# Kernel tuning notes

Hardware: AMD Instinct MI355X
Metric: run time of the kernel (lower is better)

The kernel has to match this reference:

```python
import jax, jax.numpy as jnp
import numpy as np

B, N, D = 256, 50, 128
N_NODE, MAX_ATTR = 50000, 2000
ALPHA = 0.2  # LeakyReLU negative slope
STDV = 1.0 / np.sqrt(D)  # reset_parameters uniform(-stdv, stdv)
NEG = -9e15


def setup_inputs() -> dict:
    key = jax.random.key(0)
    ks = jax.random.split(key, 10)
    uni = lambda k, shp: jax.random.uniform(k, shp, jnp.float32, -STDV, STDV)
    return {
        "inputs": jax.random.randint(ks[0], (B, N), 0, N_NODE),
        "adj": jax.random.randint(ks[1], (B, N, N), 0, 5),
        "mask_item": jax.random.randint(ks[2], (B, N), 0, 2),
        "A_attr_sess": jax.random.normal(ks[3], (B, MAX_ATTR), jnp.float32),
        "embedding": uni(ks[4], (N_NODE, D)),
        "attr_embedding": uni(ks[5], (MAX_ATTR, D)),
        "a0": uni(ks[6], (D,)),
        "a1": uni(ks[7], (D,)),
        "a2": uni(ks[8], (D,)),
        "a3": uni(ks[9], (D,)),
    }


def reference(inputs, adj, mask_item, A_attr_sess, embedding, attr_embedding, a0, a1, a2, a3):
    h = embedding[inputs]  # [B, N, D]
    # (h.repeat(1,1,N) * h.repeat(1,N,1)).view(B,N,N,D) == outer elementwise product h_i * h_j
    a_in = jax.nn.leaky_relu(h[:, :, None, :] * h[:, None, :, :], ALPHA)  # [B,N,N,D]
    a_all = jnp.stack([a0, a1, a2, a3], axis=-1)  # [D, 4]
    e = jnp.einsum('bijd,dk->bijk', a_in, a_all)  # [B,N,N,4]
    alpha = jnp.full(adj.shape, NEG, dtype=e.dtype)
    alpha = jnp.where(adj == 1, e[..., 0], alpha)
    alpha = jnp.where(adj == 2, e[..., 1], alpha)
    alpha = jnp.where(adj == 3, e[..., 2], alpha)
    alpha = jnp.where(adj == 4, e[..., 3], alpha)
    alpha = jax.nn.softmax(alpha, axis=-1)
    output = jnp.einsum('bij,bjd->bid', alpha, h)  # [B, N, D]
    attr_sess = A_attr_sess @ attr_embedding  # [B, D]
    return output, attr_sess
```

## Files before the change

### kernel.cpp

```cpp
#include <hip/hip_runtime.h>
#include <math.h>

#define BB 256
#define NN 50
#define DD 128
#define MAXA 2000
#define NEGV -9e15f
#define NATTR 256

#define H_S   136
#define HT_S  72
#define AL_S  72

#define H_OFF   0
#define HT_OFF  (64 * H_S)
#define AL_OFF  (HT_OFF + 128 * HT_S)
#define ADJ_OFF (AL_OFF + 64 * AL_S)
#define LDS_US  (ADJ_OFF + 64 * 64)

typedef __attribute__((ext_vector_type(8))) short        s8b;
typedef __attribute__((ext_vector_type(4))) float        f32x4;
typedef __attribute__((ext_vector_type(4))) unsigned int u32x4;

static __device__ __forceinline__ unsigned int pack2(float lo, float hi) {
    unsigned int r;
    asm("v_cvt_pk_bf16_f32 %0, %1, %2" : "=v"(r) : "v"(lo), "v"(hi));
    return r;
}
static __device__ __forceinline__ float bf2f(unsigned int s) {
    return __uint_as_float(s << 16);
}
static __device__ __forceinline__ f32x4 mfma16(u32x4 a, u32x4 b, f32x4 c) {
    return __builtin_amdgcn_mfma_f32_16x16x32_bf16(
        __builtin_bit_cast(s8b, a), __builtin_bit_cast(s8b, b), c, 0, 0, 0);
}

__global__ __launch_bounds__(256) void sg_fused_kernel(
    const int* __restrict__ inputs,
    const int* __restrict__ adj,
    const float* __restrict__ A_attr,
    const float* __restrict__ embedding,
    const float* __restrict__ attr_emb,
    const float* __restrict__ a0,
    const float* __restrict__ a1,
    const float* __restrict__ a2,
    const float* __restrict__ a3,
    float* __restrict__ out,
    float* __restrict__ ws)
{
    __shared__ __align__(16) unsigned short sh[LDS_US];
    const int blk  = blockIdx.x;
    const int tid  = threadIdx.x;
    const int w    = tid >> 6;
    const int lane = tid & 63;
    const int g    = lane >> 4;
    const int c    = lane & 15;
    const int goff = g * 8;

    if (blk < BB) {
        const int b = blk;

        const int  i_   = lane;
        const bool live = (i_ < NN);
        int node = 0;
        if (live) node = inputs[b * NN + i_];
        float4 gv[8];
        #pragma unroll
        for (int n = 0; n < 8; ++n) {
            gv[n] = make_float4(0.f, 0.f, 0.f, 0.f);
            if (live) gv[n] = *(const float4*)(embedding + (size_t)node * DD + (w * 8 + n) * 4);
        }
        for (int idx = tid; idx < 4096; idx += 256) {
            const int i = idx >> 6, j = idx & 63;
            int a = 0;
            if (i < NN && j < NN) a = adj[(size_t)b * (NN * NN) + i * NN + j];
            sh[ADJ_OFF + idx] = (unsigned short)a;
        }
        #pragma unroll
        for (int n = 0; n < 8; ++n) {
            const int d4 = w * 8 + n;
            const unsigned int pk01 = pack2(gv[n].x, gv[n].y);
            const unsigned int pk23 = pack2(gv[n].z, gv[n].w);
            *(uint2*)(sh + H_OFF + i_ * H_S + d4 * 4) = make_uint2(pk01, pk23);
            sh[HT_OFF + (d4 * 4 + 0) * HT_S + i_] = (unsigned short)pk01;
            sh[HT_OFF + (d4 * 4 + 1) * HT_S + i_] = (unsigned short)(pk01 >> 16);
            sh[HT_OFF + (d4 * 4 + 2) * HT_S + i_] = (unsigned short)pk23;
            sh[HT_OFF + (d4 * 4 + 3) * HT_S + i_] = (unsigned short)(pk23 >> 16);
        }
        __syncthreads();

        u32x4 hA[4];
        #pragma unroll
        for (int dt = 0; dt < 4; ++dt)
            hA[dt] = *(const u32x4*)(const void*)(sh + H_OFF + (w * 16 + c) * H_S + dt * 32 + goff);

        f32x4 accS[4][4];
        #pragma unroll
        for (int jt = 0; jt < 4; ++jt)
            #pragma unroll
            for (int k = 0; k < 4; ++k) accS[jt][k] = (f32x4){0.f, 0.f, 0.f, 0.f};

        #pragma unroll
        for (int dt = 0; dt < 4; ++dt) {
            float hf8[8], hb8[8];
            #pragma unroll
            for (int p = 0; p < 4; ++p) {
                const unsigned int hp = hA[dt][p];
                hf8[2 * p]     = bf2f(hp & 0xffffu);
                hf8[2 * p + 1] = bf2f(hp >> 16);
                hb8[2 * p]     = fabsf(hf8[2 * p]);
                hb8[2 * p + 1] = fabsf(hf8[2 * p + 1]);
            }
            u32x4 U[4], V[4];
            #pragma unroll
            for (int k = 0; k < 4; ++k) {
                const float* ap = (k == 0) ? a0 : (k == 1) ? a1 : (k == 2) ? a2 : a3;
                const float4 aL = *(const float4*)(ap + dt * 32 + goff);
                const float4 aH = *(const float4*)(ap + dt * 32 + goff + 4);
                const float a8[8] = {aL.x, aL.y, aL.z, aL.w, aH.x, aH.y, aH.z, aH.w};
                #pragma unroll
                for (int p = 0; p < 4; ++p) {
                    U[k][p] = pack2(0.6f * a8[2 * p] * hf8[2 * p],
                                    0.6f * a8[2 * p + 1] * hf8[2 * p + 1]);
                    V[k][p] = pack2(0.4f * a8[2 * p] * hb8[2 * p],
                                    0.4f * a8[2 * p + 1] * hb8[2 * p + 1]);
                }
            }
            #pragma unroll
            for (int jt = 0; jt < 4; ++jt) {
                const u32x4 hB = *(const u32x4*)(const void*)(sh + H_OFF + (jt * 16 + c) * H_S + dt * 32 + goff);
                u32x4 hBa;
                #pragma unroll
                for (int p = 0; p < 4; ++p) hBa[p] = hB[p] & 0x7fff7fffu;
                #pragma unroll
                for (int k = 0; k < 4; ++k) {
                    accS[jt][k] = mfma16(U[k], hB,  accS[jt][k]);
                    accS[jt][k] = mfma16(V[k], hBa, accS[jt][k]);
                }
            }
        }

        float s_[4][4];
        #pragma unroll
        for (int jt = 0; jt < 4; ++jt) {
            #pragma unroll
            for (int reg = 0; reg < 4; ++reg) {
                const int il = w * 16 + g * 4 + reg;
                const int j  = jt * 16 + c;
                const int a  = (int)sh[ADJ_OFF + il * 64 + j];
                float sv = (a == 1) ? accS[jt][0][reg] : (a == 2) ? accS[jt][1][reg]
                         : (a == 3) ? accS[jt][2][reg] : (a == 4) ? accS[jt][3][reg] : NEGV;
                if (j >= NN) sv = -INFINITY;
                s_[jt][reg] = sv;
            }
        }
        #pragma unroll
        for (int reg = 0; reg < 4; ++reg) {
            float m = fmaxf(fmaxf(s_[0][reg], s_[1][reg]), fmaxf(s_[2][reg], s_[3][reg]));
            m = fmaxf(m, __shfl_xor(m, 1));
            m = fmaxf(m, __shfl_xor(m, 2));
            m = fmaxf(m, __shfl_xor(m, 4));
            m = fmaxf(m, __shfl_xor(m, 8));
            const float p0 = __expf(s_[0][reg] - m);
            const float p1 = __expf(s_[1][reg] - m);
            const float p2 = __expf(s_[2][reg] - m);
            const float p3 = __expf(s_[3][reg] - m);
            float sum = (p0 + p1) + (p2 + p3);
            sum += __shfl_xor(sum, 1);
            sum += __shfl_xor(sum, 2);
            sum += __shfl_xor(sum, 4);
            sum += __shfl_xor(sum, 8);
            const float r  = 1.0f / sum;
            const int  il  = w * 16 + g * 4 + reg;
            sh[AL_OFF + il * AL_S +  0 + c] = (unsigned short)pack2(p0 * r, p0 * r);
            sh[AL_OFF + il * AL_S + 16 + c] = (unsigned short)pack2(p1 * r, p1 * r);
            sh[AL_OFF + il * AL_S + 32 + c] = (unsigned short)pack2(p2 * r, p2 * r);
            sh[AL_OFF + il * AL_S + 48 + c] = (unsigned short)pack2(p3 * r, p3 * r);
        }

        const int il = w * 16 + c;
        const u32x4 pa0 = *(const u32x4*)(const void*)(sh + AL_OFF + il * AL_S + goff);
        const u32x4 pa1 = *(const u32x4*)(const void*)(sh + AL_OFF + il * AL_S + 32 + goff);
        #pragma unroll
        for (int nt = 0; nt < 8; ++nt) {
            const u32x4 v0 = *(const u32x4*)(const void*)(sh + HT_OFF + (nt * 16 + c) * HT_S + goff);
            const u32x4 v1 = *(const u32x4*)(const void*)(sh + HT_OFF + (nt * 16 + c) * HT_S + 32 + goff);
            f32x4 accp = (f32x4){0.f, 0.f, 0.f, 0.f};
            accp = mfma16(pa0, v0, accp);
            accp = mfma16(pa1, v1, accp);
            #pragma unroll
            for (int reg = 0; reg < 4; ++reg) {
                const int ig = w * 16 + g * 4 + reg;
                if (ig < NN)
                    out[((size_t)b * NN + ig) * DD + nt * 16 + c] = accp[reg];
            }
        }
    } else {
        const int ablk = blk - BB;
        const int mg = ablk >> 4;
        const int ks = ablk & 15;
        const int m0 = mg * 16;
        const int wd = w * 32;
        const float* Arow = A_attr + (size_t)(m0 + c) * MAXA;

        const int k0 = (ks +  0) * 32;
        const int k1 = (ks + 16) * 32;
        const int k2 = (ks + 32) * 32;
        const int k3 = (ks + 48) * 32;
        const bool has3 = (ks < 15);
        const bool gd3  = (ks == 14);

        const float4 aL0 = *(const float4*)(Arow + k0 + goff);
        const float4 aH0 = *(const float4*)(Arow + k0 + goff + 4);
        const float4 aL1 = *(const float4*)(Arow + k1 + goff);
        const float4 aH1 = *(const float4*)(Arow + k1 + goff + 4);
        const float4 aL2 = *(const float4*)(Arow + k2 + goff);
        const float4 aH2 = *(const float4*)(Arow + k2 + goff + 4);
        float4 aL3 = make_float4(0.f, 0.f, 0.f, 0.f);
        float4 aH3 = make_float4(0.f, 0.f, 0.f, 0.f);
        if (has3) {
            if (!gd3 || k3 + goff + 3 < MAXA) aL3 = *(const float4*)(Arow + k3 + goff);
            if (!gd3 || k3 + goff + 7 < MAXA) aH3 = *(const float4*)(Arow + k3 + goff + 4);
        }
        float ev0[2][8], ev1[2][8], ev2[2][8], ev3[2][8];
        #pragma unroll
        for (int ntl = 0; ntl < 2; ++ntl) {
            const int col = wd + ntl * 16 + c;
            #pragma unroll
            for (int p = 0; p < 8; ++p) {
                ev0[ntl][p] = attr_emb[(size_t)(k0 + goff + p) * DD + col];
                ev1[ntl][p] = attr_emb[(size_t)(k1 + goff + p) * DD + col];
                ev2[ntl][p] = attr_emb[(size_t)(k2 + goff + p) * DD + col];
                const int kr = k3 + goff + p;
                ev3[ntl][p] = (has3 && (!gd3 || kr < MAXA))
                                  ? attr_emb[(size_t)kr * DD + col] : 0.f;
            }
        }
        f32x4 acc2[2];
        acc2[0] = (f32x4){0.f, 0.f, 0.f, 0.f};
        acc2[1] = (f32x4){0.f, 0.f, 0.f, 0.f};
        #define ATTR_CHUNK(AL, AH, EV)                                              \
        {                                                                           \
            u32x4 af;                                                               \
            af[0] = pack2(AL.x, AL.y); af[1] = pack2(AL.z, AL.w);                   \
            af[2] = pack2(AH.x, AH.y); af[3] = pack2(AH.z, AH.w);                   \
            _Pragma("unroll")                                                       \
            for (int ntl = 0; ntl < 2; ++ntl) {                                     \
                u32x4 bf_;                                                          \
                bf_[0] = pack2(EV[ntl][0], EV[ntl][1]);                             \
                bf_[1] = pack2(EV[ntl][2], EV[ntl][3]);                             \
                bf_[2] = pack2(EV[ntl][4], EV[ntl][5]);                             \
                bf_[3] = pack2(EV[ntl][6], EV[ntl][7]);                             \
                acc2[ntl] = mfma16(af, bf_, acc2[ntl]);                             \
            }                                                                       \
        }
        ATTR_CHUNK(aL0, aH0, ev0)
        ATTR_CHUNK(aL1, aH1, ev1)
        ATTR_CHUNK(aL2, aH2, ev2)
        ATTR_CHUNK(aL3, aH3, ev3)
        #undef ATTR_CHUNK

        float* pt = ws + (size_t)ablk * (16 * DD);
        #pragma unroll
        for (int ntl = 0; ntl < 2; ++ntl)
            #pragma unroll
            for (int reg = 0; reg < 4; ++reg)
                pt[(g * 4 + reg) * DD + wd + ntl * 16 + c] = acc2[ntl][reg];
    }
}

__global__ __launch_bounds__(256) void attr_reduce_kernel(
    const float* __restrict__ ws, float* __restrict__ attr_out)
{
    const int idx = blockIdx.x * 256 + threadIdx.x;
    const int m  = idx >> 5;
    const int d4 = idx & 31;
    const int mg = m >> 4;
    const int r  = m & 15;
    const float4* base = (const float4*)ws + (size_t)(mg * 16) * 512 + r * 32 + d4;
    float4 v = make_float4(0.f, 0.f, 0.f, 0.f);
    #pragma unroll
    for (int ks = 0; ks < 16; ++ks) {
        const float4 t = base[(size_t)ks * 512];
        v.x += t.x; v.y += t.y; v.z += t.z; v.w += t.w;
    }
    ((float4*)attr_out)[(size_t)m * 32 + d4] = v;
}

extern "C" void kernel_launch(void* const* d_in, const int* in_sizes, int n_in,
                              void* d_out, int out_size, void* d_ws, size_t ws_size,
                              hipStream_t stream) {
    const int*   inputs    = (const int*)  d_in[0];
    const int*   adj       = (const int*)  d_in[1];
    const float* A_attr    = (const float*)d_in[3];
    const float* embedding = (const float*)d_in[4];
    const float* attr_emb  = (const float*)d_in[5];
    const float* a0        = (const float*)d_in[6];
    const float* a1        = (const float*)d_in[7];
    const float* a2        = (const float*)d_in[8];
    const float* a3        = (const float*)d_in[9];

    float* out      = (float*)d_out;
    float* attr_out = out + (size_t)BB * NN * DD;
    float* ws       = (float*)d_ws;

    sg_fused_kernel<<<BB + NATTR, 256, 0, stream>>>(inputs, adj, A_attr, embedding,
                                                    attr_emb, a0, a1, a2, a3,
                                                    out, ws);
    attr_reduce_kernel<<<32, 256, 0, stream>>>(ws, attr_out);
}
```

Baseline: 20.50 us.

## Split each batch's attention rows across two blocks to double GAT parallelism

The attention part now launches two blocks per batch element instead of one. Each block redundantly loads the embeddings and adjacency into LDS, then only two of its four waves compute their 16-row tiles. Half-empty blocks then exit early. The aim is to spread the MFMA and softmax work over more CUs and shorten the per-block critical path, at the cost of duplicated gathers and LDS staging, and idle waves during the load phase. The pack2 asm output also gets an early-clobber constraint.

After: 22.65 us. 1.1x slower.

```diff
diff --git a/kernel.cpp b/kernel.cpp
--- a/kernel.cpp
+++ b/kernel.cpp
@@ -6,6 +6,7 @@
 #define DD 128
 #define MAXA 2000
 #define NEGV -9e15f
+#define NGAT  512
 #define NATTR 256
 
 #define H_S   136
@@ -24,7 +25,7 @@
 
 static __device__ __forceinline__ unsigned int pack2(float lo, float hi) {
     unsigned int r;
-    asm("v_cvt_pk_bf16_f32 %0, %1, %2" : "=v"(r) : "v"(lo), "v"(hi));
+    asm("v_cvt_pk_bf16_f32 %0, %1, %2" : "=&v"(r) : "v"(lo), "v"(hi));
     return r;
 }
 static __device__ __forceinline__ float bf2f(unsigned int s) {
@@ -57,8 +58,9 @@
     const int c    = lane & 15;
     const int goff = g * 8;
 
-    if (blk < BB) {
-        const int b = blk;
+    if (blk < NGAT) {
+        const int b = blk & 255;
+        const int p = blk >> 8;
 
         const int  i_   = lane;
         const bool live = (i_ < NN);
@@ -89,10 +91,13 @@
         }
         __syncthreads();
 
+        if (w >= 2) return;
+        const int T = 2 * p + w;
+
         u32x4 hA[4];
         #pragma unroll
         for (int dt = 0; dt < 4; ++dt)
-            hA[dt] = *(const u32x4*)(const void*)(sh + H_OFF + (w * 16 + c) * H_S + dt * 32 + goff);
+            hA[dt] = *(const u32x4*)(const void*)(sh + H_OFF + (T * 16 + c) * H_S + dt * 32 + goff);
 
         f32x4 accS[4][4];
         #pragma unroll
@@ -104,12 +109,12 @@
         for (int dt = 0; dt < 4; ++dt) {
             float hf8[8], hb8[8];
             #pragma unroll
-            for (int p = 0; p < 4; ++p) {
-                const unsigned int hp = hA[dt][p];
-                hf8[2 * p]     = bf2f(hp & 0xffffu);
-                hf8[2 * p + 1] = bf2f(hp >> 16);
-                hb8[2 * p]     = fabsf(hf8[2 * p]);
-                hb8[2 * p + 1] = fabsf(hf8[2 * p + 1]);
+            for (int q = 0; q < 4; ++q) {
+                const unsigned int hp = hA[dt][q];
+                hf8[2 * q]     = bf2f(hp & 0xffffu);
+                hf8[2 * q + 1] = bf2f(hp >> 16);
+                hb8[2 * q]     = fabsf(hf8[2 * q]);
+                hb8[2 * q + 1] = fabsf(hf8[2 * q + 1]);
             }
             u32x4 U[4], V[4];
             #pragma unroll
@@ -119,11 +124,11 @@
                 const float4 aH = *(const float4*)(ap + dt * 32 + goff + 4);
                 const float a8[8] = {aL.x, aL.y, aL.z, aL.w, aH.x, aH.y, aH.z, aH.w};
                 #pragma unroll
-                for (int p = 0; p < 4; ++p) {
-                    U[k][p] = pack2(0.6f * a8[2 * p] * hf8[2 * p],
-                                    0.6f * a8[2 * p + 1] * hf8[2 * p + 1]);
-                    V[k][p] = pack2(0.4f * a8[2 * p] * hb8[2 * p],
-                                    0.4f * a8[2 * p + 1] * hb8[2 * p + 1]);
+                for (int q = 0; q < 4; ++q) {
+                    U[k][q] = pack2(0.6f * a8[2 * q] * hf8[2 * q],
+                                    0.6f * a8[2 * q + 1] * hf8[2 * q + 1]);
+                    V[k][q] = pack2(0.4f * a8[2 * q] * hb8[2 * q],
+                                    0.4f * a8[2 * q + 1] * hb8[2 * q + 1]);
                 }
             }
             #pragma unroll
@@ -131,7 +136,7 @@
                 const u32x4 hB = *(const u32x4*)(const void*)(sh + H_OFF + (jt * 16 + c) * H_S + dt * 32 + goff);
                 u32x4 hBa;
                 #pragma unroll
-                for (int p = 0; p < 4; ++p) hBa[p] = hB[p] & 0x7fff7fffu;
+                for (int q = 0; q < 4; ++q) hBa[q] = hB[q] & 0x7fff7fffu;
                 #pragma unroll
                 for (int k = 0; k < 4; ++k) {
                     accS[jt][k] = mfma16(U[k], hB,  accS[jt][k]);
@@ -145,7 +150,7 @@
         for (int jt = 0; jt < 4; ++jt) {
             #pragma unroll
             for (int reg = 0; reg < 4; ++reg) {
-                const int il = w * 16 + g * 4 + reg;
+                const int il = T * 16 + g * 4 + reg;
                 const int j  = jt * 16 + c;
                 const int a  = (int)sh[ADJ_OFF + il * 64 + j];
                 float sv = (a == 1) ? accS[jt][0][reg] : (a == 2) ? accS[jt][1][reg]
@@ -171,14 +176,14 @@
             sum += __shfl_xor(sum, 4);
             sum += __shfl_xor(sum, 8);
             const float r  = 1.0f / sum;
-            const int  il  = w * 16 + g * 4 + reg;
+            const int  il  = T * 16 + g * 4 + reg;
             sh[AL_OFF + il * AL_S +  0 + c] = (unsigned short)pack2(p0 * r, p0 * r);
             sh[AL_OFF + il * AL_S + 16 + c] = (unsigned short)pack2(p1 * r, p1 * r);
             sh[AL_OFF + il * AL_S + 32 + c] = (unsigned short)pack2(p2 * r, p2 * r);
             sh[AL_OFF + il * AL_S + 48 + c] = (unsigned short)pack2(p3 * r, p3 * r);
         }
 
-        const int il = w * 16 + c;
+        const int il = T * 16 + c;
         const u32x4 pa0 = *(const u32x4*)(const void*)(sh + AL_OFF + il * AL_S + goff);
         const u32x4 pa1 = *(const u32x4*)(const void*)(sh + AL_OFF + il * AL_S + 32 + goff);
         #pragma unroll
@@ -190,13 +195,13 @@
             accp = mfma16(pa1, v1, accp);
             #pragma unroll
             for (int reg = 0; reg < 4; ++reg) {
-                const int ig = w * 16 + g * 4 + reg;
+                const int ig = T * 16 + g * 4 + reg;
                 if (ig < NN)
                     out[((size_t)b * NN + ig) * DD + nt * 16 + c] = accp[reg];
             }
         }
     } else {
-        const int ablk = blk - BB;
+        const int ablk = blk - NGAT;
         const int mg = ablk >> 4;
         const int ks = ablk & 15;
         const int m0 = mg * 16;
@@ -304,8 +309,8 @@
     float* attr_out = out + (size_t)BB * NN * DD;
     float* ws       = (float*)d_ws;
 
-    sg_fused_kernel<<<BB + NATTR, 256, 0, stream>>>(inputs, adj, A_attr, embedding,
-                                                    attr_emb, a0, a1, a2, a3,
-                                                    out, ws);
+    sg_fused_kernel<<<NGAT + NATTR, 256, 0, stream>>>(inputs, adj, A_attr, embedding,
+                                                      attr_emb, a0, a1, a2, a3,
+                                                      out, ws);
     attr_reduce_kernel<<<32, 256, 0, stream>>>(ws, attr_out);
 }
```
